# Performance work log

Measured on AMD Instinct MI355X. Metric: run time of the kernel, lower is better.

Reference implementation:

```python
import jax, jax.numpy as jnp
import numpy as np

NPERSEG = 1024
NOVERLAP = 768
STEP = NPERSEG - NOVERLAP  # 256
BATCH = 1024
SEQ_LEN = 16384


def setup_inputs() -> dict:
    key = jax.random.key(0)
    k1, k2, k3, k4 = jax.random.split(key, 4)
    inp = jax.random.normal(k1, (BATCH, SEQ_LEN), dtype=jnp.float32)
    freqs = jax.random.uniform(k2, (NPERSEG,), dtype=jnp.float32)  # learned freq params
    fc_w = jax.random.normal(k3, (1, 1), dtype=jnp.float32)
    fc_b = jax.random.normal(k4, (1,), dtype=jnp.float32)
    return {"input": inp, "freqs": freqs, "fc_w": fc_w, "fc_b": fc_b}


def reference(input, freqs, fc_w, fc_b):
    B, S = input.shape
    nwin = (S - NPERSEG) // STEP + 1  # number of overlapping windows
    # gather all windows at once: [nwin, NPERSEG] index grid
    idx = jnp.arange(nwin)[:, None] * STEP + jnp.arange(NPERSEG)[None, :]
    win = input[:, idx]  # [B, nwin, NPERSEG]
    # complex weights v = exp(-2*pi*i*freqs), applied as real/imag parts
    ang = (2.0 * jnp.pi) * freqs
    re = jnp.einsum('bwp,p->bw', win, jnp.cos(ang))   # Re(x . v)
    im = jnp.einsum('bwp,p->bw', win, -jnp.sin(ang))  # Im(x . v)
    # mean over windows, then |.|^2
    fr = jnp.mean(re, axis=1)
    fi = jnp.mean(im, axis=1)
    psd = (fr * fr + fi * fi)[:, None]  # [B, 1]
    # Linear(1,1)
    return psd @ fc_w.T + fc_b
```

## Files before the change

### kernel.cpp

```cpp
#include <hip/hip_runtime.h>
#include <math.h>

#define NPERSEG 1024
#define STEP    256
#define NWIN    61
#define SEQ     16384
#define BATCH   1024

__global__ void welch_weights_kernel(const float* __restrict__ freqs,
                                     float* __restrict__ wc,
                                     float* __restrict__ ws) {
    int s = blockIdx.x * blockDim.x + threadIdx.x;
    if (s >= SEQ) return;
    int p0    = s & (STEP - 1);
    int wbase = s >> 8;
    float c = 0.f, sn = 0.f;
    #pragma unroll
    for (int k = 0; k < 4; ++k) {
        int w = wbase - k;
        if (w >= 0 && w < NWIN) {
            int p = p0 + STEP * k;
            float a = 6.2831853071795864769f * freqs[p];
            float sv, cv;
            sincosf(a, &sv, &cv);
            c  += cv;
            sn -= sv;
        }
    }
    wc[s] = c;
    ws[s] = sn;
}

__global__ __launch_bounds__(256, 4) void welch_dot_kernel(
        const float* __restrict__ inp,
        const float* __restrict__ wc,
        const float* __restrict__ ws,
        const float* __restrict__ fc_w,
        const float* __restrict__ fc_b,
        float* __restrict__ out) {
    const int row = blockIdx.x;
    const int t   = threadIdx.x;

    const float4* __restrict__ x4  = (const float4*)(inp + (size_t)row * SEQ);
    const float4* __restrict__ wc4 = (const float4*)wc;
    const float4* __restrict__ ws4 = (const float4*)ws;

    float sr = 0.f, si = 0.f;
    #pragma unroll 4
    for (int i = 0; i < SEQ / 4 / 256; ++i) {
        int j = t + i * 256;
        float4 xv = x4[j];
        float4 cv = wc4[j];
        float4 sv = ws4[j];
        sr += xv.x * cv.x + xv.y * cv.y + xv.z * cv.z + xv.w * cv.w;
        si += xv.x * sv.x + xv.y * sv.y + xv.z * sv.z + xv.w * sv.w;
    }

    #pragma unroll
    for (int off = 32; off > 0; off >>= 1) {
        sr += __shfl_down(sr, off, 64);
        si += __shfl_down(si, off, 64);
    }

    __shared__ float red[8];
    int wave = t >> 6;
    int lane = t & 63;
    if (lane == 0) { red[wave * 2] = sr; red[wave * 2 + 1] = si; }
    __syncthreads();

    if (t == 0) {
        float fr = 0.f, fi = 0.f;
        #pragma unroll
        for (int w = 0; w < 4; ++w) { fr += red[w * 2]; fi += red[w * 2 + 1]; }
        fr *= (1.0f / NWIN);
        fi *= (1.0f / NWIN);
        out[row] = (fr * fr + fi * fi) * fc_w[0] + fc_b[0];
    }
}

extern "C" void kernel_launch(void* const* d_in, const int* in_sizes, int n_in,
                              void* d_out, int out_size, void* d_ws, size_t ws_size,
                              hipStream_t stream) {
    const float* inp   = (const float*)d_in[0];
    const float* freqs = (const float*)d_in[1];
    const float* fc_w  = (const float*)d_in[2];
    const float* fc_b  = (const float*)d_in[3];
    float* out = (float*)d_out;

    float* wc = (float*)d_ws;
    float* ws = wc + SEQ;

    welch_weights_kernel<<<SEQ / 256, 256, 0, stream>>>(freqs, wc, ws);
    welch_dot_kernel<<<BATCH, 256, 0, stream>>>(inp, wc, ws, fc_w, fc_b, out);
}
```

Before: 101.4 us.

## Process two rows per block, reusing weight loads, with nontemporal input loads

Each block now computes two batch rows, so each loaded cos/sin weight vector is used for two input rows, halving weight traffic per row. Input loads use nontemporal hints so the streamed input is less likely to evict the reused weights from cache. The 1/NWIN scaling moves into the weight precompute kernel. The grid is halved to 512 blocks and launch bounds drop to 2, which may lower occupancy and the number of loads in flight on a bandwidth-bound kernel.

Result: slower. 106.2 us (+4.7%).

```diff
diff --git a/kernel.cpp b/kernel.cpp
--- a/kernel.cpp
+++ b/kernel.cpp
@@ -6,6 +6,8 @@
 #define NWIN    61
 #define SEQ     16384
 #define BATCH   1024
+
+typedef float f32x4 __attribute__((ext_vector_type(4)));
 
 __global__ void welch_weights_kernel(const float* __restrict__ freqs,
                                      float* __restrict__ wc,
@@ -27,54 +29,66 @@
             sn -= sv;
         }
     }
-    wc[s] = c;
-    ws[s] = sn;
+    wc[s] = c  * (1.0f / NWIN);
+    ws[s] = sn * (1.0f / NWIN);
 }
 
-__global__ __launch_bounds__(256, 4) void welch_dot_kernel(
+__global__ __launch_bounds__(256, 2) void welch_dot2_kernel(
         const float* __restrict__ inp,
         const float* __restrict__ wc,
         const float* __restrict__ ws,
         const float* __restrict__ fc_w,
         const float* __restrict__ fc_b,
         float* __restrict__ out) {
-    const int row = blockIdx.x;
-    const int t   = threadIdx.x;
+    const int r0 = blockIdx.x * 2;
+    const int t  = threadIdx.x;
 
-    const float4* __restrict__ x4  = (const float4*)(inp + (size_t)row * SEQ);
-    const float4* __restrict__ wc4 = (const float4*)wc;
-    const float4* __restrict__ ws4 = (const float4*)ws;
+    const f32x4* __restrict__ xa  = (const f32x4*)(inp + (size_t)r0 * SEQ);
+    const f32x4* __restrict__ xb  = (const f32x4*)(inp + (size_t)(r0 + 1) * SEQ);
+    const f32x4* __restrict__ wc4 = (const f32x4*)wc;
+    const f32x4* __restrict__ ws4 = (const f32x4*)ws;
 
-    float sr = 0.f, si = 0.f;
+    float sra = 0.f, sia = 0.f, srb = 0.f, sib = 0.f;
     #pragma unroll 4
     for (int i = 0; i < SEQ / 4 / 256; ++i) {
         int j = t + i * 256;
-        float4 xv = x4[j];
-        float4 cv = wc4[j];
-        float4 sv = ws4[j];
-        sr += xv.x * cv.x + xv.y * cv.y + xv.z * cv.z + xv.w * cv.w;
-        si += xv.x * sv.x + xv.y * sv.y + xv.z * sv.z + xv.w * sv.w;
+        f32x4 cv = wc4[j];
+        f32x4 sv = ws4[j];
+        f32x4 a  = __builtin_nontemporal_load(xa + j);
+        f32x4 b  = __builtin_nontemporal_load(xb + j);
+        sra += a.x * cv.x + a.y * cv.y + a.z * cv.z + a.w * cv.w;
+        sia += a.x * sv.x + a.y * sv.y + a.z * sv.z + a.w * sv.w;
+        srb += b.x * cv.x + b.y * cv.y + b.z * cv.z + b.w * cv.w;
+        sib += b.x * sv.x + b.y * sv.y + b.z * sv.z + b.w * sv.w;
     }
 
     #pragma unroll
     for (int off = 32; off > 0; off >>= 1) {
-        sr += __shfl_down(sr, off, 64);
-        si += __shfl_down(si, off, 64);
+        sra += __shfl_down(sra, off, 64);
+        sia += __shfl_down(sia, off, 64);
+        srb += __shfl_down(srb, off, 64);
+        sib += __shfl_down(sib, off, 64);
     }
 
-    __shared__ float red[8];
+    __shared__ float red[4][4];
     int wave = t >> 6;
     int lane = t & 63;
-    if (lane == 0) { red[wave * 2] = sr; red[wave * 2 + 1] = si; }
+    if (lane == 0) {
+        red[wave][0] = sra; red[wave][1] = sia;
+        red[wave][2] = srb; red[wave][3] = sib;
+    }
     __syncthreads();
 
     if (t == 0) {
-        float fr = 0.f, fi = 0.f;
+        float fra = 0.f, fia = 0.f, frb = 0.f, fib = 0.f;
         #pragma unroll
-        for (int w = 0; w < 4; ++w) { fr += red[w * 2]; fi += red[w * 2 + 1]; }
-        fr *= (1.0f / NWIN);
-        fi *= (1.0f / NWIN);
-        out[row] = (fr * fr + fi * fi) * fc_w[0] + fc_b[0];
+        for (int w = 0; w < 4; ++w) {
+            fra += red[w][0]; fia += red[w][1];
+            frb += red[w][2]; fib += red[w][3];
+        }
+        float fw = fc_w[0], fb = fc_b[0];
+        out[r0]     = (fra * fra + fia * fia) * fw + fb;
+        out[r0 + 1] = (frb * frb + fib * fib) * fw + fb;
     }
 }
 
@@ -91,5 +105,5 @@
     float* ws = wc + SEQ;
 
     welch_weights_kernel<<<SEQ / 256, 256, 0, stream>>>(freqs, wc, ws);
-    welch_dot_kernel<<<BATCH, 256, 0, stream>>>(inp, wc, ws, fc_w, fc_b, out);
+    welch_dot2_kernel<<<BATCH / 2, 256, 0, stream>>>(inp, wc, ws, fc_w, fc_b, out);
 }
```

## Fuse weight computation into dot kernel using periodic weight structure

Applied to the files above, without the earlier changes.

Removes the separate weights kernel and the global weight arrays. Each thread computes its 4 positions' folded cos/sin weights in registers, relying on the fact that interior positions (s in [1024, 15360)) all share the same full 4-term sum since STEP=256 is the per-thread stride. Only the first and last chunks use prefix/suffix partial sums. This drops one launch and the weight loads from the streaming loop, at the cost of 16 sincosf per thread in every block.

New measurement: 98.80 us. 2.6% less time.

```diff
diff --git a/kernel.cpp b/kernel.cpp
--- a/kernel.cpp
+++ b/kernel.cpp
@@ -7,53 +7,58 @@
 #define SEQ     16384
 #define BATCH   1024
 
-__global__ void welch_weights_kernel(const float* __restrict__ freqs,
-                                     float* __restrict__ wc,
-                                     float* __restrict__ ws) {
-    int s = blockIdx.x * blockDim.x + threadIdx.x;
-    if (s >= SEQ) return;
-    int p0    = s & (STEP - 1);
-    int wbase = s >> 8;
-    float c = 0.f, sn = 0.f;
-    #pragma unroll
-    for (int k = 0; k < 4; ++k) {
-        int w = wbase - k;
-        if (w >= 0 && w < NWIN) {
-            int p = p0 + STEP * k;
-            float a = 6.2831853071795864769f * freqs[p];
-            float sv, cv;
-            sincosf(a, &sv, &cv);
-            c  += cv;
-            sn -= sv;
-        }
-    }
-    wc[s] = c;
-    ws[s] = sn;
-}
+typedef float f32x4 __attribute__((ext_vector_type(4)));
 
-__global__ __launch_bounds__(256, 4) void welch_dot_kernel(
+__global__ __launch_bounds__(256, 4) void welch_fused_kernel(
         const float* __restrict__ inp,
-        const float* __restrict__ wc,
-        const float* __restrict__ ws,
+        const float* __restrict__ freqs,
         const float* __restrict__ fc_w,
         const float* __restrict__ fc_b,
         float* __restrict__ out) {
     const int row = blockIdx.x;
     const int t   = threadIdx.x;
 
-    const float4* __restrict__ x4  = (const float4*)(inp + (size_t)row * SEQ);
-    const float4* __restrict__ wc4 = (const float4*)wc;
-    const float4* __restrict__ ws4 = (const float4*)ws;
+    float Fc[4], Fs[4], Pc[4], Ps[4], Sc[4], Ss[4];
+    #pragma unroll
+    for (int e = 0; e < 4; ++e) {
+        int idx = 4 * t + e;
+        int p0  = idx & 255;
+        int q   = idx >> 8;
+        float fc_ = 0.f, fs_ = 0.f, pc_ = 0.f, ps_ = 0.f, sc_ = 0.f, ss_ = 0.f;
+        #pragma unroll
+        for (int k = 0; k < 4; ++k) {
+            float a = 6.2831853071795864769f * freqs[p0 + 256 * k];
+            float sv, cv;
+            sincosf(a, &sv, &cv);
+            cv *= (1.0f / NWIN);
+            sv *= -(1.0f / NWIN);
+            fc_ += cv; fs_ += sv;
+            if (k <= q) { pc_ += cv; ps_ += sv; }
+            if (k >= q) { sc_ += cv; ss_ += sv; }
+        }
+        Fc[e] = fc_; Fs[e] = fs_;
+        Pc[e] = pc_; Ps[e] = ps_;
+        Sc[e] = sc_; Ss[e] = ss_;
+    }
+
+    const f32x4* __restrict__ x4 = (const f32x4*)(inp + (size_t)row * SEQ);
 
     float sr = 0.f, si = 0.f;
-    #pragma unroll 4
-    for (int i = 0; i < SEQ / 4 / 256; ++i) {
-        int j = t + i * 256;
-        float4 xv = x4[j];
-        float4 cv = wc4[j];
-        float4 sv = ws4[j];
-        sr += xv.x * cv.x + xv.y * cv.y + xv.z * cv.z + xv.w * cv.w;
-        si += xv.x * sv.x + xv.y * sv.y + xv.z * sv.z + xv.w * sv.w;
+    {
+        f32x4 x = x4[t];
+        sr += x.x * Pc[0] + x.y * Pc[1] + x.z * Pc[2] + x.w * Pc[3];
+        si += x.x * Ps[0] + x.y * Ps[1] + x.z * Ps[2] + x.w * Ps[3];
+    }
+    #pragma unroll 7
+    for (int i = 1; i < 15; ++i) {
+        f32x4 x = x4[t + 256 * i];
+        sr += x.x * Fc[0] + x.y * Fc[1] + x.z * Fc[2] + x.w * Fc[3];
+        si += x.x * Fs[0] + x.y * Fs[1] + x.z * Fs[2] + x.w * Fs[3];
+    }
+    {
+        f32x4 x = x4[t + 256 * 15];
+        sr += x.x * Sc[0] + x.y * Sc[1] + x.z * Sc[2] + x.w * Sc[3];
+        si += x.x * Ss[0] + x.y * Ss[1] + x.z * Ss[2] + x.w * Ss[3];
     }
 
     #pragma unroll
@@ -62,18 +67,15 @@
         si += __shfl_down(si, off, 64);
     }
 
-    __shared__ float red[8];
+    __shared__ float red[4][2];
     int wave = t >> 6;
     int lane = t & 63;
-    if (lane == 0) { red[wave * 2] = sr; red[wave * 2 + 1] = si; }
+    if (lane == 0) { red[wave][0] = sr; red[wave][1] = si; }
     __syncthreads();
 
     if (t == 0) {
-        float fr = 0.f, fi = 0.f;
-        #pragma unroll
-        for (int w = 0; w < 4; ++w) { fr += red[w * 2]; fi += red[w * 2 + 1]; }
-        fr *= (1.0f / NWIN);
-        fi *= (1.0f / NWIN);
+        float fr = red[0][0] + red[1][0] + red[2][0] + red[3][0];
+        float fi = red[0][1] + red[1][1] + red[2][1] + red[3][1];
         out[row] = (fr * fr + fi * fi) * fc_w[0] + fc_b[0];
     }
 }
@@ -87,9 +89,5 @@
     const float* fc_b  = (const float*)d_in[3];
     float* out = (float*)d_out;
 
-    float* wc = (float*)d_ws;
-    float* ws = wc + SEQ;
-
-    welch_weights_kernel<<<SEQ / 256, 256, 0, stream>>>(freqs, wc, ws);
-    welch_dot_kernel<<<BATCH, 256, 0, stream>>>(inp, wc, ws, fc_w, fc_b, out);
+    welch_fused_kernel<<<BATCH, 256, 0, stream>>>(inp, freqs, fc_w, fc_b, out);
 }
```
